# Kernel tuning notes

Hardware: AMD Instinct MI355X
Metric: run time of the kernel (lower is better)

## Reference

```python
import jax, jax.numpy as jnp
import numpy as np

B, H, W, C = 4, 128, 128, 256
D_MODEL, NH = 512, 8
DH = D_MODEL // NH  # 64


def setup_inputs() -> dict:
    key = jax.random.key(0)
    ks = jax.random.split(key, 5)
    s = lambda fan_in: 1.0 / np.sqrt(fan_in)
    return {
        "x": jax.random.normal(ks[0], (B, H, W, C), jnp.float32),
        "Wq": jax.random.normal(ks[1], (C, D_MODEL), jnp.float32) * s(C),
        "bq": jnp.zeros((D_MODEL,), jnp.float32),
        "Wk": jax.random.normal(ks[2], (C, D_MODEL), jnp.float32) * s(C),
        "bk": jnp.zeros((D_MODEL,), jnp.float32),
        "Wv": jax.random.normal(ks[3], (C, D_MODEL), jnp.float32) * s(C),
        "bv": jnp.zeros((D_MODEL,), jnp.float32),
        "Wo": jax.random.normal(ks[4], (D_MODEL, C), jnp.float32) * s(D_MODEL),
        "bo": jnp.zeros((C,), jnp.float32),
    }


def reference(x, Wq, bq, Wk, bk, Wv, bv, Wo, bo):
    # Axial multi-head attention along axis 1 (H), W axis is batched.
    b, h, w, _ = x.shape
    q = (x @ Wq + bq).reshape(b, h, w, NH, DH) * (DH ** -0.5)
    k = (x @ Wk + bk).reshape(b, h, w, NH, DH)
    v = (x @ Wv + bv).reshape(b, h, w, NH, DH)
    # scores over the H axis: [B, Nh, W, H, H]
    scores = jnp.einsum("bxwnd,bywnd->bnwxy", q, k)
    probs = jax.nn.softmax(scores, axis=-1)
    # [B, H, W, Nh, DH] -> [B, H, W, d_model]
    out = jnp.einsum("bnwxy,bywnd->bxwnd", probs, v).reshape(b, h, w, D_MODEL)
    # Wo projection; original combines to [B,W,H,C] then permutes back to [B,H,W,C],
    # which is equivalent to applying Wo directly here. Dropout is identity at inference.
    return out @ Wo + bo
```

## Files before the change

### kernel.cpp

```cpp
#include <hip/hip_runtime.h>

typedef unsigned short u16;
typedef __attribute__((ext_vector_type(8))) short bf16x8;
typedef __attribute__((ext_vector_type(8))) unsigned short u16x8;
typedef __attribute__((ext_vector_type(4))) unsigned u32x4;
typedef __attribute__((ext_vector_type(4))) float f32x4;

#define DEVI static __device__ __forceinline__

DEVI u16 f2b(float f) {
  unsigned u = __builtin_bit_cast(unsigned, f);
  return (u16)((u + 0x7FFFu + ((u >> 16) & 1u)) >> 16);
}

DEVI unsigned cvtpk(float a, float b) {
  unsigned r;
  asm("v_cvt_pk_bf16_f32 %0, %1, %2" : "=v"(r) : "v"(a), "v"(b));
  return r;
}

DEVI void gload_lds16(const void* g, void* l) {
  __builtin_amdgcn_global_load_lds(
      (const __attribute__((address_space(1))) unsigned int*)g,
      (__attribute__((address_space(3))) unsigned int*)l, 16, 0, 0);
}


__global__ __launch_bounds__(256) void prep_x(const float* __restrict__ x, u16* __restrict__ xb) {
  const int n8 = 65536 * 256 / 8;
  int i = blockIdx.x * blockDim.x + threadIdx.x;
  for (; i < n8; i += gridDim.x * blockDim.x) {
    const float4* p = (const float4*)x + (size_t)i * 2;
    float4 a = p[0], b = p[1];
    u16x8 r;
    r[0] = f2b(a.x); r[1] = f2b(a.y); r[2] = f2b(a.z); r[3] = f2b(a.w);
    r[4] = f2b(b.x); r[5] = f2b(b.y); r[6] = f2b(b.z); r[7] = f2b(b.w);
    *(u16x8*)(xb + (size_t)i * 8) = r;
  }
}

__global__ __launch_bounds__(256) void prep_w(
    const float* __restrict__ Wq, const float* __restrict__ Wk,
    const float* __restrict__ Wv, const float* __restrict__ Wo,
    const float* __restrict__ bq, const float* __restrict__ bk, const float* __restrict__ bv,
    u16* __restrict__ wqkvT, u16* __restrict__ woT, float* __restrict__ bqkv) {
  const int NW1 = 1536 * 256, NW2 = 256 * 512;
  const int total = NW1 + NW2 + 1536;
  int i = blockIdx.x * blockDim.x + threadIdx.x;
  for (; i < total; i += gridDim.x * blockDim.x) {
    if (i < NW1) {
      int nn = i >> 8, kk = i & 255;
      float v;
      if (nn < 512)       v = Wq[kk * 512 + nn] * 0.125f;
      else if (nn < 1024) v = Wk[kk * 512 + (nn - 512)];
      else                v = Wv[kk * 512 + (nn - 1024)];
      wqkvT[i] = f2b(v);
    } else if (i < NW1 + NW2) {
      int j = i - NW1;
      int nn = j >> 9, kk = j & 511;
      woT[j] = f2b(Wo[kk * 256 + nn]);
    } else {
      int j = i - NW1 - NW2;
      bqkv[j] = (j < 512) ? bq[j] * 0.125f : (j < 1024 ? bk[j - 512] : bv[j - 1024]);
    }
  }
}


template <int KK, int OMODE>
__global__ __launch_bounds__(1024) void gemm256(
    const u16* __restrict__ A, const u16* __restrict__ Bt,
    const float* __restrict__ bias, void* __restrict__ Cv, int N) {
  constexpr int NT = KK / 64;
  __shared__ u16 smem[65536];
  const int tid = threadIdx.x;
  const int lane = tid & 63, wid = tid >> 6;
  const int nTn = N >> 8;
  const int qx = gridDim.x >> 3;
  const int wg = (blockIdx.x & 7) * qx + (blockIdx.x >> 3);
  const long m0 = (long)(wg / nTn) * 256;
  const long n0 = (long)(wg % nTn) * 256;
  const int wr = wid >> 2, wc = wid & 3;
  const int hi = lane >> 4, lo = lane & 15;
  const u16* Ab = A + m0 * KK;
  const u16* Bb = Bt + n0 * KK;
  const int srow_ = tid >> 3;
  const int schunk = tid & 7;

  f32x4 acc[4][4];
#pragma unroll
  for (int mi = 0; mi < 4; ++mi)
#pragma unroll
    for (int ni = 0; ni < 4; ++ni) acc[mi][ni] = f32x4{0.f, 0.f, 0.f, 0.f};

  auto stage = [&](int t) {
    u16* base = &smem[(t & 1) * 32768];
    const int kt = t * 64;
#pragma unroll
    for (int j = 0; j < 2; ++j) {
      int row = j * 128 + srow_;
      int colE = (schunk ^ (row & 7)) << 3;
      gload_lds16(Ab + (long)row * KK + kt + colE, &base[(j * 1024 + tid) * 8]);
    }
#pragma unroll
    for (int j = 0; j < 2; ++j) {
      int row = j * 128 + srow_;
      int colE = (schunk ^ (row & 7)) << 3;
      gload_lds16(Bb + (long)row * KK + kt + colE, &base[16384 + (j * 1024 + tid) * 8]);
    }
  };

  stage(0);
#pragma unroll
  for (int t = 0; t < NT; ++t) {
    if (t + 1 < NT) {
      stage(t + 1);
      asm volatile("s_waitcnt vmcnt(4)" ::: "memory");
    } else {
      asm volatile("s_waitcnt vmcnt(0)" ::: "memory");
    }
    __builtin_amdgcn_sched_barrier(0);
    __builtin_amdgcn_s_barrier();
    const u16* aB = &smem[(t & 1) * 32768];
    const u16* bB = aB + 16384;
#pragma unroll
    for (int ks = 0; ks < 2; ++ks) {
      const int slot = ((hi + ks * 4) ^ (lo & 7)) << 3;
      bf16x8 af[4], bfr[4];
#pragma unroll
      for (int mi = 0; mi < 4; ++mi)
        af[mi] = *(const bf16x8*)&aB[(wr * 64 + mi * 16 + lo) * 64 + slot];
#pragma unroll
      for (int ni = 0; ni < 4; ++ni)
        bfr[ni] = *(const bf16x8*)&bB[(wc * 64 + ni * 16 + lo) * 64 + slot];
#pragma unroll
      for (int mi = 0; mi < 4; ++mi)
#pragma unroll
        for (int ni = 0; ni < 4; ++ni)
          acc[mi][ni] = __builtin_amdgcn_mfma_f32_16x16x32_bf16(af[mi], bfr[ni], acc[mi][ni], 0, 0, 0);
    }
    __builtin_amdgcn_sched_barrier(0);
    __builtin_amdgcn_s_barrier();
  }

  float bb[4];
#pragma unroll
  for (int ni = 0; ni < 4; ++ni) bb[ni] = bias[n0 + wc * 64 + ni * 16 + lo];

  if (OMODE == 2) {
    u16* Cg = (u16*)Cv;
#pragma unroll
    for (int mi = 0; mi < 4; ++mi)
#pragma unroll
      for (int ni = 0; ni < 4; ++ni) {
#pragma unroll
        for (int j = 0; j < 4; ++j) {
          int row = wr * 64 + mi * 16 + hi * 4 + j;
          int chunk = (wc * 8 + ni * 2 + (lo >> 3)) ^ ((row >> 2) & 7);
          smem[row * 256 + chunk * 8 + (lo & 7)] = f2b(acc[mi][ni][j] + bb[ni]);
        }
      }
    __syncthreads();
#pragma unroll
    for (int it = 0; it < 8; ++it) {
      int idx = it * 1024 + tid;
      int row = idx >> 5, c = idx & 31;
      int cs = c ^ ((row >> 2) & 7);
      long m = m0 + row;
      int col = (int)n0 + c * 8;
      int b_ = (int)(m >> 14), yw = (int)m & 16383;
      int y = yw >> 7, w = yw & 127;
      int t = col >> 9, h = (col >> 6) & 7, dh = col & 63;
      size_t dst = ((((size_t)(b_ * 128 + w) * 8 + h) * 3 + t) * 128 + y) * 64 + dh;
      *(u16x8*)(Cg + dst) = *(const u16x8*)&smem[row * 256 + cs * 8];
    }
  } else {
    float* Cg = (float*)Cv;
#pragma unroll
    for (int mi = 0; mi < 4; ++mi)
#pragma unroll
      for (int ni = 0; ni < 4; ++ni) {
        long cg = n0 + wc * 64 + ni * 16 + lo;
#pragma unroll
        for (int j = 0; j < 4; ++j)
          Cg[(m0 + wr * 64 + mi * 16 + hi * 4 + j) * N + cg] = acc[mi][ni][j] + bb[ni];
      }
  }
}


__global__ __launch_bounds__(256, 5) void attn_axial(const u16* __restrict__ qkv,
                                                     u16* __restrict__ ao) {
  __shared__ u16 smem[16384];
  u16* kld = smem;
  u16* vt  = smem + 8192;

  const int g = blockIdx.x;
  const int n = g & 7, w = (g >> 3) & 127, b = g >> 10;
  const int tid = threadIdx.x, lane = tid & 63, wid = tid >> 6;
  const size_t pq = (((size_t)(b * 128 + w) * 8 + n) * 3) * 8192;
  const u16* Qp = qkv + pq;
  const u16* Kp = qkv + pq + 8192;
  const u16* Vp = qkv + pq + 16384;
  const int hi = lane >> 4, lo = lane & 15;

  {
    const int kr0 = tid >> 3, kc = tid & 7;
#pragma unroll
    for (int i = 0; i < 4; ++i) {
      const int row = i * 32 + kr0;
      const int srcC = (kc ^ (row & 7)) << 3;
      gload_lds16(Kp + row * 64 + srcC, &kld[(i * 256 + tid) * 8]);
    }
  }

  const int vyp = (tid & 63) * 2;
  const u16* vg = Vp + vyp * 64 + wid * 16;
  u16x8 va0 = *(const u16x8*)vg;
  u16x8 va1 = *(const u16x8*)(vg + 8);
  u16x8 vc0 = *(const u16x8*)(vg + 64);
  u16x8 vc1 = *(const u16x8*)(vg + 72);

  bf16x8 qf[2][2];
#pragma unroll
  for (int cg = 0; cg < 2; ++cg)
#pragma unroll
    for (int ks = 0; ks < 2; ++ks)
      qf[cg][ks] = *(const bf16x8*)(Qp + (wid * 32 + cg * 16 + lo) * 64 + hi * 8 + ks * 32);

  {
    unsigned* vt32 = (unsigned*)vt;
    const int cch = vyp >> 3;
    const int cw = (vyp >> 1) & 3;
#pragma unroll
    for (int e = 0; e < 8; ++e) {
      const int d0 = wid * 16 + e, d1 = wid * 16 + 8 + e;
      const int c0s = (cch & 8) | ((cch & 7) ^ (d0 & 7));
      const int c1s = (cch & 8) | ((cch & 7) ^ (d1 & 7));
      vt32[d0 * 64 + c0s * 4 + cw] = (unsigned)va0[e] | ((unsigned)vc0[e] << 16);
      vt32[d1 * 64 + c1s * 4 + cw] = (unsigned)va1[e] | ((unsigned)vc1[e] << 16);
    }
  }

  __syncthreads();

  f32x4 s2[2][8];
#pragma unroll
  for (int cg = 0; cg < 2; ++cg)
#pragma unroll
    for (int ni = 0; ni < 8; ++ni) s2[cg][ni] = f32x4{0.f, 0.f, 0.f, 0.f};
  __builtin_amdgcn_s_setprio(1);
#pragma unroll
  for (int ks = 0; ks < 2; ++ks)
#pragma unroll
    for (int ni = 0; ni < 8; ++ni) {
      const int kr = ni * 16 + lo;
      bf16x8 kf = *(const bf16x8*)&kld[kr * 64 + (((hi + ks * 4) ^ (kr & 7)) << 3)];
      s2[0][ni] = __builtin_amdgcn_mfma_f32_16x16x32_bf16(kf, qf[0][ks], s2[0][ni], 0, 0, 0);
      s2[1][ni] = __builtin_amdgcn_mfma_f32_16x16x32_bf16(kf, qf[1][ks], s2[1][ni], 0, 0, 0);
    }
  __builtin_amdgcn_s_setprio(0);

  unsigned setA[2][4][2], setB[2][4][2];
#pragma unroll
  for (int cg = 0; cg < 2; ++cg) {
    float mx = s2[cg][0][0];
#pragma unroll
    for (int ni = 0; ni < 8; ++ni)
#pragma unroll
      for (int j = 0; j < 4; ++j) mx = fmaxf(mx, s2[cg][ni][j]);
    mx = fmaxf(mx, __shfl_xor(mx, 16, 64));
    mx = fmaxf(mx, __shfl_xor(mx, 32, 64));
    float sum = 0.f;
#pragma unroll
    for (int ni = 0; ni < 8; ++ni)
#pragma unroll
      for (int j = 0; j < 4; ++j) {
        float e = exp2f((s2[cg][ni][j] - mx) * 1.44269504f);
        s2[cg][ni][j] = e;
        sum += e;
      }
    sum += __shfl_xor(sum, 16, 64);
    sum += __shfl_xor(sum, 32, 64);
    const float r = 1.f / sum;

    unsigned pkE[4][2], pkO[4][2];
#pragma unroll
    for (int o = 0; o < 4; ++o) {
      pkE[o][0] = cvtpk(s2[cg][2 * o][0] * r, s2[cg][2 * o][1] * r);
      pkE[o][1] = cvtpk(s2[cg][2 * o][2] * r, s2[cg][2 * o][3] * r);
      pkO[o][0] = cvtpk(s2[cg][2 * o + 1][0] * r, s2[cg][2 * o + 1][1] * r);
      pkO[o][1] = cvtpk(s2[cg][2 * o + 1][2] * r, s2[cg][2 * o + 1][3] * r);
    }
    const bool lowHi = (hi < 2);
    unsigned keepR[4][2], gotR[4][2];
#pragma unroll
    for (int o = 0; o < 4; ++o)
#pragma unroll
      for (int e = 0; e < 2; ++e) {
        unsigned snd = lowHi ? pkO[o][e] : pkE[o][e];
        keepR[o][e] = lowHi ? pkE[o][e] : pkO[o][e];
        gotR[o][e] = __shfl_xor(snd, 32, 64);
      }
    const bool fwdGot = (hi == 0) || (hi == 3);
    unsigned recv2[4][2];
#pragma unroll
    for (int o = 0; o < 4; ++o)
#pragma unroll
      for (int e = 0; e < 2; ++e) {
        unsigned snd = fwdGot ? gotR[o][e] : keepR[o][e];
        recv2[o][e] = __shfl_xor(snd, 16, 64);
      }
#pragma unroll
    for (int o = 0; o < 4; ++o)
#pragma unroll
      for (int e = 0; e < 2; ++e) {
        setA[cg][o][e] = (hi & 1) ? recv2[o][e] : (hi == 0 ? keepR[o][e] : gotR[o][e]);
        setB[cg][o][e] = (hi & 1) ? (hi == 1 ? gotR[o][e] : keepR[o][e]) : recv2[o][e];
      }
  }

  f32x4 o2[2][4];
#pragma unroll
  for (int cg = 0; cg < 2; ++cg)
#pragma unroll
    for (int ni = 0; ni < 4; ++ni) o2[cg][ni] = f32x4{0.f, 0.f, 0.f, 0.f};
  __builtin_amdgcn_s_setprio(1);
#pragma unroll
  for (int ks = 0; ks < 4; ++ks) {
    const int cch = hi + ks * 4;
    bf16x8 pa[2];
#pragma unroll
    for (int cg = 0; cg < 2; ++cg) {
      u32x4 t;
      t[0] = setA[cg][ks][0]; t[1] = setA[cg][ks][1];
      t[2] = setB[cg][ks][0]; t[3] = setB[cg][ks][1];
      pa[cg] = __builtin_bit_cast(bf16x8, t);
    }
#pragma unroll
    for (int ni = 0; ni < 4; ++ni) {
      const int vr = ni * 16 + lo;
      const int cs = (cch & 8) | ((cch & 7) ^ (vr & 7));
      bf16x8 vf = *(const bf16x8*)&vt[vr * 128 + cs * 8];
      o2[0][ni] = __builtin_amdgcn_mfma_f32_16x16x32_bf16(pa[0], vf, o2[0][ni], 0, 0, 0);
      o2[1][ni] = __builtin_amdgcn_mfma_f32_16x16x32_bf16(pa[1], vf, o2[1][ni], 0, 0, 0);
    }
  }
  __builtin_amdgcn_s_setprio(0);

#pragma unroll
  for (int cg = 0; cg < 2; ++cg)
#pragma unroll
    for (int j = 0; j < 4; ++j) {
      const int q = wid * 32 + cg * 16 + hi * 4 + j;
      const size_t obase = ((size_t)(b * 16384 + q * 128 + w)) * 512 + (size_t)n * 64;
#pragma unroll
      for (int ni = 0; ni < 4; ++ni)
        ao[obase + ni * 16 + lo] = f2b(o2[cg][ni][j]);
    }
}


extern "C" void kernel_launch(void* const* d_in, const int* in_sizes, int n_in,
                              void* d_out, int out_size, void* d_ws, size_t ws_size,
                              hipStream_t stream) {
  (void)in_sizes; (void)n_in; (void)out_size; (void)ws_size;
  const float* x  = (const float*)d_in[0];
  const float* Wq = (const float*)d_in[1];
  const float* bq = (const float*)d_in[2];
  const float* Wk = (const float*)d_in[3];
  const float* bk = (const float*)d_in[4];
  const float* Wv = (const float*)d_in[5];
  const float* bv = (const float*)d_in[6];
  const float* Wo = (const float*)d_in[7];
  const float* bo = (const float*)d_in[8];
  float* out = (float*)d_out;

  char* ws = (char*)d_ws;
  const size_t MiB = (size_t)1 << 20;
  u16* qkv   = (u16*)ws;
  u16* xb    = (u16*)(ws + 192 * MiB);
  u16* wqkvT = (u16*)(ws + 224 * MiB);
  u16* woT   = wqkvT + 1536 * 256;
  float* bqkv = (float*)(woT + 256 * 512);

  prep_x<<<2048, 256, 0, stream>>>(x, xb);
  prep_w<<<512, 256, 0, stream>>>(Wq, Wk, Wv, Wo, bq, bk, bv, wqkvT, woT, bqkv);

  gemm256<256, 2><<<1536, 1024, 0, stream>>>(xb, wqkvT, bqkv, qkv, 1536);
  attn_axial<<<4096, 256, 0, stream>>>(qkv, (u16*)out);
  gemm256<512, 0><<<256, 1024, 0, stream>>>((const u16*)out, woT, bo, out, 256);
}
```

Baseline: 210.4 us.

## Replace QKV GEMM with column-tiled kernel writing per-column attention panels directly

The bf16 conversion of x now writes it transposed to [B,W,H,C], so each column (b,w) is one contiguous 128x256 tile. A new gemmcol kernel keeps that A tile in registers, streams the QKV weights through double-buffered LDS with global_load_lds, and writes Q/K/V results straight into a per-column panel layout [b,w][t*8+head][y][dh]. This removes the LDS-staged scatter epilogue of the old 256x256 GEMM, and the attention kernel's addressing is updated to match. The trade-off is a 4x64 A-tile register footprint, smaller 128-wide N tiles, and 8-byte scattered output stores.

```diff
diff --git a/kernel.cpp b/kernel.cpp
--- a/kernel.cpp
+++ b/kernel.cpp
@@ -3,6 +3,7 @@
 typedef unsigned short u16;
 typedef __attribute__((ext_vector_type(8))) short bf16x8;
 typedef __attribute__((ext_vector_type(8))) unsigned short u16x8;
+typedef __attribute__((ext_vector_type(4))) unsigned short u16x4;
 typedef __attribute__((ext_vector_type(4))) unsigned u32x4;
 typedef __attribute__((ext_vector_type(4))) float f32x4;
 
@@ -26,7 +27,7 @@
 }
 
 
-__global__ __launch_bounds__(256) void prep_x(const float* __restrict__ x, u16* __restrict__ xb) {
+__global__ __launch_bounds__(256) void prep_x2(const float* __restrict__ x, u16* __restrict__ xb2) {
   const int n8 = 65536 * 256 / 8;
   int i = blockIdx.x * blockDim.x + threadIdx.x;
   for (; i < n8; i += gridDim.x * blockDim.x) {
@@ -35,7 +36,9 @@
     u16x8 r;
     r[0] = f2b(a.x); r[1] = f2b(a.y); r[2] = f2b(a.z); r[3] = f2b(a.w);
     r[4] = f2b(b.x); r[5] = f2b(b.y); r[6] = f2b(b.z); r[7] = f2b(b.w);
-    *(u16x8*)(xb + (size_t)i * 8) = r;
+    const int t = i >> 5, c0 = (i & 31) * 8;
+    const int b_ = t >> 14, y = (t >> 7) & 127, w = t & 127;
+    *(u16x8*)(xb2 + (((size_t)(b_ * 128 + w) * 128) + y) * 256 + c0) = r;
   }
 }
 
@@ -67,7 +70,105 @@
 }
 
 
-template <int KK, int OMODE>
+__global__ __launch_bounds__(256) void gemmcol(
+    const u16* __restrict__ xb2, const u16* __restrict__ Bt,
+    const float* __restrict__ bias, u16* __restrict__ Cg) {
+  __shared__ u16 blds[16384];
+  const int tid = threadIdx.x, lane = tid & 63, wid = tid >> 6;
+  const int lo = lane & 15, hi = lane >> 4;
+  const int wr = wid >> 1, wc = wid & 1;
+  const int ct = blockIdx.x;
+  const u16* Xp = xb2 + (size_t)ct * 32768;
+  const int srow = tid >> 3, schunk = tid & 7;
+  const size_t pbase = (size_t)ct * 24 * 8192;
+
+  bf16x8 areg[4][8];
+#pragma unroll
+  for (int yT = 0; yT < 4; ++yT)
+#pragma unroll
+    for (int ks = 0; ks < 8; ++ks)
+      areg[yT][ks] = *(const bf16x8*)(Xp + (wr * 64 + yT * 16 + lo) * 256 + hi * 8 + ks * 32);
+
+  auto stageB = [&](int j2, int t2) {
+    u16* dst = &blds[(t2 & 1) * 8192];
+    const u16* src = Bt + (size_t)(j2 * 128) * 256 + t2 * 64;
+#pragma unroll
+    for (int q = 0; q < 4; ++q) {
+      const int row = q * 32 + srow;
+      const int colE = (schunk ^ (row & 7)) << 3;
+      gload_lds16(src + (size_t)row * 256 + colE, &dst[(q * 256 + tid) * 8]);
+    }
+  };
+
+  f32x4 acc[4][4];
+#pragma unroll
+  for (int nI = 0; nI < 4; ++nI)
+#pragma unroll
+    for (int mI = 0; mI < 4; ++mI) acc[nI][mI] = f32x4{0.f, 0.f, 0.f, 0.f};
+
+  stageB(0, 0);
+  for (int j = 0; j < 12; ++j) {
+#pragma unroll
+    for (int t = 0; t < 4; ++t) {
+      if (t == 0) {
+        stageB(j, 1);
+        if (j == 0) { asm volatile("s_waitcnt vmcnt(4)" ::: "memory"); }
+        else        { asm volatile("s_waitcnt vmcnt(20)" ::: "memory"); }
+      } else if (t < 3) {
+        stageB(j, t + 1);
+        asm volatile("s_waitcnt vmcnt(4)" ::: "memory");
+      } else if (j < 11) {
+        stageB(j + 1, 0);
+        asm volatile("s_waitcnt vmcnt(4)" ::: "memory");
+      } else {
+        asm volatile("s_waitcnt vmcnt(0)" ::: "memory");
+      }
+      __builtin_amdgcn_sched_barrier(0);
+      __builtin_amdgcn_s_barrier();
+      const u16* bB = &blds[(t & 1) * 8192];
+#pragma unroll
+      for (int ks2 = 0; ks2 < 2; ++ks2) {
+        bf16x8 bfr[4];
+#pragma unroll
+        for (int nI = 0; nI < 4; ++nI) {
+          const int nrow = wc * 64 + nI * 16 + lo;
+          bfr[nI] = *(const bf16x8*)&bB[nrow * 64 + (((ks2 * 4 + hi) ^ (nrow & 7)) << 3)];
+        }
+#pragma unroll
+        for (int nI = 0; nI < 4; ++nI)
+#pragma unroll
+          for (int mI = 0; mI < 4; ++mI)
+            acc[nI][mI] = __builtin_amdgcn_mfma_f32_16x16x32_bf16(
+                bfr[nI], areg[mI][t * 2 + ks2], acc[nI][mI], 0, 0, 0);
+      }
+      __builtin_amdgcn_sched_barrier(0);
+      __builtin_amdgcn_s_barrier();
+    }
+
+    const int n0 = j * 128;
+#pragma unroll
+    for (int nI = 0; nI < 4; ++nI) {
+      const int col0 = n0 + wc * 64 + nI * 16 + hi * 4;
+      const float4 bb = *(const float4*)&bias[col0];
+      u16* pan = Cg + pbase + (size_t)((col0 >> 9) * 8 + ((col0 >> 6) & 7)) * 8192;
+      const int dh0 = col0 & 63;
+#pragma unroll
+      for (int mI = 0; mI < 4; ++mI) {
+        const int y = wr * 64 + mI * 16 + lo;
+        u16x4 pk;
+        pk[0] = f2b(acc[nI][mI][0] + bb.x);
+        pk[1] = f2b(acc[nI][mI][1] + bb.y);
+        pk[2] = f2b(acc[nI][mI][2] + bb.z);
+        pk[3] = f2b(acc[nI][mI][3] + bb.w);
+        *(u16x4*)&pan[y * 64 + dh0] = pk;
+        acc[nI][mI] = f32x4{0.f, 0.f, 0.f, 0.f};
+      }
+    }
+  }
+}
+
+
+template <int KK>
 __global__ __launch_bounds__(1024) void gemm256(
     const u16* __restrict__ A, const u16* __restrict__ Bt,
     const float* __restrict__ bias, void* __restrict__ Cv, int N) {
@@ -147,45 +248,16 @@
 #pragma unroll
   for (int ni = 0; ni < 4; ++ni) bb[ni] = bias[n0 + wc * 64 + ni * 16 + lo];
 
-  if (OMODE == 2) {
-    u16* Cg = (u16*)Cv;
-#pragma unroll
-    for (int mi = 0; mi < 4; ++mi)
-#pragma unroll
-      for (int ni = 0; ni < 4; ++ni) {
-#pragma unroll
-        for (int j = 0; j < 4; ++j) {
-          int row = wr * 64 + mi * 16 + hi * 4 + j;
-          int chunk = (wc * 8 + ni * 2 + (lo >> 3)) ^ ((row >> 2) & 7);
-          smem[row * 256 + chunk * 8 + (lo & 7)] = f2b(acc[mi][ni][j] + bb[ni]);
-        }
-      }
-    __syncthreads();
-#pragma unroll
-    for (int it = 0; it < 8; ++it) {
-      int idx = it * 1024 + tid;
-      int row = idx >> 5, c = idx & 31;
-      int cs = c ^ ((row >> 2) & 7);
-      long m = m0 + row;
-      int col = (int)n0 + c * 8;
-      int b_ = (int)(m >> 14), yw = (int)m & 16383;
-      int y = yw >> 7, w = yw & 127;
-      int t = col >> 9, h = (col >> 6) & 7, dh = col & 63;
-      size_t dst = ((((size_t)(b_ * 128 + w) * 8 + h) * 3 + t) * 128 + y) * 64 + dh;
-      *(u16x8*)(Cg + dst) = *(const u16x8*)&smem[row * 256 + cs * 8];
-    }
-  } else {
-    float* Cg = (float*)Cv;
-#pragma unroll
-    for (int mi = 0; mi < 4; ++mi)
-#pragma unroll
-      for (int ni = 0; ni < 4; ++ni) {
-        long cg = n0 + wc * 64 + ni * 16 + lo;
-#pragma unroll
-        for (int j = 0; j < 4; ++j)
-          Cg[(m0 + wr * 64 + mi * 16 + hi * 4 + j) * N + cg] = acc[mi][ni][j] + bb[ni];
-      }
-  }
+  float* Cg = (float*)Cv;
+#pragma unroll
+  for (int mi = 0; mi < 4; ++mi)
+#pragma unroll
+    for (int ni = 0; ni < 4; ++ni) {
+      long cg = n0 + wc * 64 + ni * 16 + lo;
+#pragma unroll
+      for (int j = 0; j < 4; ++j)
+        Cg[(m0 + wr * 64 + mi * 16 + hi * 4 + j) * N + cg] = acc[mi][ni][j] + bb[ni];
+    }
 }
 
 
@@ -198,10 +270,10 @@
   const int g = blockIdx.x;
   const int n = g & 7, w = (g >> 3) & 127, b = g >> 10;
   const int tid = threadIdx.x, lane = tid & 63, wid = tid >> 6;
-  const size_t pq = (((size_t)(b * 128 + w) * 8 + n) * 3) * 8192;
-  const u16* Qp = qkv + pq;
-  const u16* Kp = qkv + pq + 8192;
-  const u16* Vp = qkv + pq + 16384;
+  const size_t pb = (size_t)(b * 128 + w) * 24 * 8192;
+  const u16* Qp = qkv + pb + (size_t)n * 8192;
+  const u16* Kp = qkv + pb + (size_t)(8 + n) * 8192;
+  const u16* Vp = qkv + pb + (size_t)(16 + n) * 8192;
   const int hi = lane >> 4, lo = lane & 15;
 
   {
@@ -379,15 +451,15 @@
   char* ws = (char*)d_ws;
   const size_t MiB = (size_t)1 << 20;
   u16* qkv   = (u16*)ws;
-  u16* xb    = (u16*)(ws + 192 * MiB);
+  u16* xb2   = (u16*)(ws + 192 * MiB);
   u16* wqkvT = (u16*)(ws + 224 * MiB);
   u16* woT   = wqkvT + 1536 * 256;
   float* bqkv = (float*)(woT + 256 * 512);
 
-  prep_x<<<2048, 256, 0, stream>>>(x, xb);
+  prep_x2<<<2048, 256, 0, stream>>>(x, xb2);
   prep_w<<<512, 256, 0, stream>>>(Wq, Wk, Wv, Wo, bq, bk, bv, wqkvT, woT, bqkv);
 
-  gemm256<256, 2><<<1536, 1024, 0, stream>>>(xb, wqkvT, bqkv, qkv, 1536);
+  gemmcol<<<512, 256, 0, stream>>>(xb2, wqkvT, bqkv, qkv);
   attn_axial<<<4096, 256, 0, stream>>>(qkv, (u16*)out);
-  gemm256<512, 0><<<256, 1024, 0, stream>>>((const u16*)out, woT, bo, out, 256);
-}
+  gemm256<512><<<256, 1024, 0, stream>>>((const u16*)out, woT, bo, out, 256);
+}
```

Result: slower. 223.1 us (+6.1%).
